# Kernel optimization log

Hardware: AMD Instinct MI355X
Metric: run time of the kernel (lower is better)

## Reference

```python
import jax, jax.numpy as jnp
import numpy as np

B, N, C, W = 128, 512, 128, 128
MASK_FILL = -1e-06  # faithful to original (sic: -1e-06, not -1e6)


def setup_inputs() -> dict:
    key = jax.random.key(0)
    ks = jax.random.split(key, 8)
    s = 1.0 / np.sqrt(C)
    return {
        "x": jax.random.normal(ks[0], (B, N, C), dtype=jnp.float32),
        "Wq": jax.random.normal(ks[1], (C, W), dtype=jnp.float32) * s,
        "bq": jnp.zeros((W,), dtype=jnp.float32),
        "Wk": jax.random.normal(ks[2], (C, W), dtype=jnp.float32) * s,
        "bk": jnp.zeros((W,), dtype=jnp.float32),
        "Wv": jax.random.normal(ks[3], (C, W), dtype=jnp.float32) * s,
        "bv": jnp.zeros((W,), dtype=jnp.float32),
        "valid_len": jax.random.randint(ks[4], (B,), 0, N, dtype=jnp.int64),
    }


def reference(x, Wq, bq, Wk, bk, Wv, bv, valid_len):
    # QKV projections: [B, N, W]
    q = jnp.einsum("bnc,cw->bnw", x, Wq) + bq
    k = jnp.einsum("bnc,cw->bnw", x, Wk) + bk
    v = jnp.einsum("bnc,cw->bnw", x, Wv) + bv
    # scores: [B, N, N]
    scores = jnp.einsum("bnw,bmw->bnm", q, k)
    # masked softmax: positions m where m > valid_len[b] get MASK_FILL
    # (mask is identical across query rows n since valid_len is per-batch)
    keep = jnp.arange(N)[None, None, :] <= valid_len[:, None, None]  # [B,1,N]
    scores = jnp.where(keep, scores, MASK_FILL)
    attn = jax.nn.softmax(scores, axis=-1)
    return jnp.einsum("bnm,bmw->bnw", attn, v)
```

## Files before the change

kernel.cpp:

```cpp
#include <hip/hip_runtime.h>
#include <hip/hip_fp16.h>
#include <math.h>

#define B_ 128
#define N_ 512
#define C_ 128
#define W_ 128
#define LDSW 136

typedef _Float16 f16;
typedef _Float16 f16x8 __attribute__((ext_vector_type(8)));
typedef _Float16 f16x4 __attribute__((ext_vector_type(4)));
typedef float f32x4 __attribute__((ext_vector_type(4)));

#define MFMA16(a, b, c) __builtin_amdgcn_mfma_f32_16x16x32_f16(a, b, c, 0, 0, 0)

#define LOG2E 1.44269504f
#define MASKF (-1e-6f * LOG2E)

static __device__ __forceinline__ f32x4 max4(f32x4 a, f32x4 b) {
  f32x4 r;
  r[0] = fmaxf(a[0], b[0]);
  r[1] = fmaxf(a[1], b[1]);
  r[2] = fmaxf(a[2], b[2]);
  r[3] = fmaxf(a[3], b[3]);
  return r;
}

__global__ __launch_bounds__(256) void prep_w(const float* __restrict__ Wq,
                                              const float* __restrict__ Wk,
                                              const float* __restrict__ Wv,
                                              f16* __restrict__ wT) {
  __shared__ float xs[16 * 129];
  const float* src = blockIdx.x == 0 ? Wq : (blockIdx.x == 1 ? Wk : Wv);
  f16* dst = wT + (size_t)blockIdx.x * C_ * W_;
  const int c0 = blockIdx.y * 16;
  const int t = threadIdx.x;
  for (int ii = 0; ii < 2; ++ii) {
    int idx = t + 256 * ii;
    int row = idx >> 5, w4 = idx & 31;
    float4 v = *reinterpret_cast<const float4*>(src + (c0 + row) * W_ + w4 * 4);
    xs[row * 129 + w4 * 4 + 0] = v.x;
    xs[row * 129 + w4 * 4 + 1] = v.y;
    xs[row * 129 + w4 * 4 + 2] = v.z;
    xs[row * 129 + w4 * 4 + 3] = v.w;
  }
  __syncthreads();
  int o = t * 8;
  int w = o >> 4, cc = o & 15;
  f16x8 h;
  for (int jj = 0; jj < 8; ++jj) h[jj] = (f16)xs[(cc + jj) * 129 + w];
  *reinterpret_cast<f16x8*>(dst + w * C_ + c0 + cc) = h;
}

__global__ __launch_bounds__(256, 2) void proj(const float* __restrict__ x,
                                               const float* __restrict__ bq,
                                               const float* __restrict__ bk,
                                               const float* __restrict__ bv,
                                               const f16* __restrict__ wT,
                                               f16* __restrict__ q,
                                               f16* __restrict__ k,
                                               f16* __restrict__ vT) {
  __shared__ f16 wls[2][128 * LDSW];
  const int b = blockIdx.y, n0 = blockIdx.x * 128;
  const int t = threadIdx.x, wave = t >> 6, lane = t & 63;
  const int quad = lane >> 4, l15 = lane & 15;

  float4 xr[2][4][2];
  for (int tile = 0; tile < 2; ++tile)
    for (int ks = 0; ks < 4; ++ks) {
      const float* p = x + ((size_t)(b * N_ + n0 + wave * 32 + tile * 16 +
                                     l15)) * C_ + ks * 32 + quad * 8;
      xr[tile][ks][0] = *reinterpret_cast<const float4*>(p);
      xr[tile][ks][1] = *reinterpret_cast<const float4*>(p + 4);
    }

  for (int i = 0; i < 8; ++i) {
    int idx = t + 256 * i;
    f16x8 tmp = *reinterpret_cast<const f16x8*>(wT + (size_t)idx * 8);
    *reinterpret_cast<f16x8*>(&wls[0][(idx >> 4) * LDSW + (idx & 15) * 8]) =
        tmp;
  }

  f16x8 af[2][4];
  for (int tile = 0; tile < 2; ++tile)
    for (int ks = 0; ks < 4; ++ks) {
      f16x8 h;
      h[0] = (f16)xr[tile][ks][0].x; h[1] = (f16)xr[tile][ks][0].y;
      h[2] = (f16)xr[tile][ks][0].z; h[3] = (f16)xr[tile][ks][0].w;
      h[4] = (f16)xr[tile][ks][1].x; h[5] = (f16)xr[tile][ks][1].y;
      h[6] = (f16)xr[tile][ks][1].z; h[7] = (f16)xr[tile][ks][1].w;
      af[tile][ks] = h;
    }
  __syncthreads();

  for (int ph = 0; ph < 3; ++ph) {
    const f16* wl = wls[ph & 1];

    f16x8 wst[8];
    if (ph < 2)
      for (int i = 0; i < 8; ++i)
        wst[i] = *reinterpret_cast<const f16x8*>(
            wT + (size_t)(ph + 1) * 16384 + (size_t)(t + 256 * i) * 8);

    f32x4 acc[8][2];
    for (int ct = 0; ct < 8; ++ct) {
      acc[ct][0] = {0.f, 0.f, 0.f, 0.f};
      acc[ct][1] = {0.f, 0.f, 0.f, 0.f};
    }

    if (ph < 2) {
      for (int ct = 0; ct < 8; ++ct) {
        f16x8 wf[4];
        for (int ks = 0; ks < 4; ++ks)
          wf[ks] = *reinterpret_cast<const f16x8*>(
              &wl[(ct * 16 + l15) * LDSW + ks * 32 + quad * 8]);
        for (int ks = 0; ks < 4; ++ks) {
          acc[ct][0] = MFMA16(wf[ks], af[0][ks], acc[ct][0]);
          acc[ct][1] = MFMA16(wf[ks], af[1][ks], acc[ct][1]);
        }
      }
      const float* bias = ph == 0 ? bq : bk;
      const float scale = ph == 0 ? LOG2E : 1.0f;
      f16* dst = ph == 0 ? q : k;
      for (int ct = 0; ct < 8; ++ct) {
        const float4 bb =
            *reinterpret_cast<const float4*>(bias + ct * 16 + quad * 4);
        for (int tile = 0; tile < 2; ++tile) {
          int n = n0 + wave * 32 + tile * 16 + l15;
          f16x4 h;
          h.x = (f16)((acc[ct][tile][0] + bb.x) * scale);
          h.y = (f16)((acc[ct][tile][1] + bb.y) * scale);
          h.z = (f16)((acc[ct][tile][2] + bb.z) * scale);
          h.w = (f16)((acc[ct][tile][3] + bb.w) * scale);
          *reinterpret_cast<f16x4*>(dst + ((size_t)(b * N_ + n)) * W_ +
                                    ct * 16 + quad * 4) = h;
        }
      }
    } else {
      for (int ct = 0; ct < 8; ++ct) {
        f16x8 wf[4];
        for (int ks = 0; ks < 4; ++ks)
          wf[ks] = *reinterpret_cast<const f16x8*>(
              &wl[(ct * 16 + l15) * LDSW + ks * 32 + quad * 8]);
        for (int ks = 0; ks < 4; ++ks) {
          acc[ct][0] = MFMA16(af[0][ks], wf[ks], acc[ct][0]);
          acc[ct][1] = MFMA16(af[1][ks], wf[ks], acc[ct][1]);
        }
      }
      for (int ct = 0; ct < 8; ++ct) {
        int wcol = ct * 16 + l15;
        float bb = bv[wcol];
        for (int tile = 0; tile < 2; ++tile) {
          int n = n0 + wave * 32 + tile * 16 + quad * 4;
          f16x4 h;
          h.x = (f16)(acc[ct][tile][0] + bb);
          h.y = (f16)(acc[ct][tile][1] + bb);
          h.z = (f16)(acc[ct][tile][2] + bb);
          h.w = (f16)(acc[ct][tile][3] + bb);
          *reinterpret_cast<f16x4*>(&vT[((size_t)(b * W_ + wcol)) * N_ + n]) =
              h;
        }
      }
    }

    if (ph < 2) {
      for (int i = 0; i < 8; ++i) {
        int idx = t + 256 * i;
        *reinterpret_cast<f16x8*>(
            &wls[(ph + 1) & 1][(idx >> 4) * LDSW + (idx & 15) * 8]) = wst[i];
      }
      __syncthreads();
    }
  }
}

__global__ __launch_bounds__(256, 2) void flash(const f16* __restrict__ q,
                                                const f16* __restrict__ k,
                                                const f16* __restrict__ vT,
                                                const int* __restrict__ vlen,
                                                float* __restrict__ out) {
  __shared__ f16 kls[128 * LDSW];
  __shared__ f16 pls[128 * LDSW];
  __shared__ float bcast[128];
  const int b = blockIdx.x, m0 = blockIdx.y * 128;
  const int t = threadIdx.x, wave = t >> 6, lane = t & 63;
  const int quad = lane >> 4, l15 = lane & 15;
  const int vl = vlen[b];
  const int mcol = m0 + wave * 32;
  const int srow = t >> 4, sc16 = t & 15;

  f16x8 qf[2][4];
  for (int ct = 0; ct < 2; ++ct)
    for (int kt = 0; kt < 4; ++kt)
      qf[ct][kt] = *reinterpret_cast<const f16x8*>(
          q + ((size_t)(b * N_ + mcol + ct * 16 + l15)) * W_ + kt * 32 +
          quad * 8);

  f32x4 oacc[2][8];
  for (int wt = 0; wt < 2; ++wt)
    for (int cm = 0; cm < 8; ++cm) oacc[wt][cm] = {0.f, 0.f, 0.f, 0.f};
  float mrun[2] = {-3.4e38f, -3.4e38f}, lrun[2] = {0.f, 0.f};

  for (int i = 0; i < 8; ++i) {
    int row = srow + 16 * i;
    f16x8 tmp = *reinterpret_cast<const f16x8*>(
        k + ((size_t)(b * N_ + row)) * W_ + sc16 * 8);
    *reinterpret_cast<f16x8*>(&kls[row * LDSW + sc16 * 8]) = tmp;
  }
  __syncthreads();

  for (int j = 0; j < 4; ++j) {
    const int n0 = j * 128;
    const int rel = vl - n0;

    f16x8 vfa[4];
    for (int kt = 0; kt < 4; ++kt)
      vfa[kt] = *reinterpret_cast<const f16x8*>(
          vT + ((size_t)(b * W_ + wave * 32 + l15)) * N_ + n0 + kt * 32 +
          quad * 8);

    f16x8 kst[8];
    if (j < 3)
      for (int i = 0; i < 8; ++i)
        kst[i] = *reinterpret_cast<const f16x8*>(
            k + ((size_t)(b * N_ + n0 + 128 + srow + 16 * i)) * W_ + sc16 * 8);

    f32x4 sacc[8][2];
    for (int i = 0; i < 8; ++i) {
      sacc[i][0] = {0.f, 0.f, 0.f, 0.f};
      sacc[i][1] = {0.f, 0.f, 0.f, 0.f};
      f16x8 kf[4];
      for (int kt = 0; kt < 4; ++kt)
        kf[kt] = *reinterpret_cast<const f16x8*>(
            &kls[(i * 16 + l15) * LDSW + kt * 32 + quad * 8]);
      for (int kt = 0; kt < 4; ++kt) {
        sacc[i][0] = MFMA16(kf[kt], qf[0][kt], sacc[i][0]);
        sacc[i][1] = MFMA16(kf[kt], qf[1][kt], sacc[i][1]);
      }
    }

    if (rel >= 0 && rel < 128) {
#pragma unroll
      for (int i = 0; i < 8; ++i) {
        if (rel >= 16 * i && rel < 16 * i + 15) {
          for (int r = 0; r < 4; ++r) {
            int nn = 16 * i + quad * 4 + r;
            if (nn > rel) { sacc[i][0][r] = MASKF; sacc[i][1][r] = MASKF; }
          }
        }
      }
    }

    float alpha[2];
    for (int ct = 0; ct < 2; ++ct) {
      f32x4 vmx = {-3.4e38f, -3.4e38f, -3.4e38f, -3.4e38f};
#pragma unroll
      for (int i = 0; i < 8; ++i)
        if (16 * i <= rel) vmx = max4(vmx, sacc[i][ct]);
      float mx = fmaxf(fmaxf(vmx[0], vmx[1]), fmaxf(vmx[2], vmx[3]));
      mx = fmaxf(mx, __shfl_xor(mx, 16));
      mx = fmaxf(mx, __shfl_xor(mx, 32));
      float mnew = fmaxf(mrun[ct], mx);
      alpha[ct] = exp2f(mrun[ct] - mnew);
      mrun[ct] = mnew;
      float pm = exp2f(MASKF - mnew);
      f32x4 vs = {0.f, 0.f, 0.f, 0.f};
      float sm = 0.f;
#pragma unroll
      for (int i = 0; i < 8; ++i) {
        if (16 * i > rel) {
          f32x4 v = {pm, pm, pm, pm};
          sacc[i][ct] = v;
          sm += 4.f * pm;
        } else {
          for (int r = 0; r < 4; ++r)
            sacc[i][ct][r] = exp2f(sacc[i][ct][r] - mnew);
          vs += sacc[i][ct];
        }
      }
      float s = (vs[0] + vs[1]) + (vs[2] + vs[3]) + sm;
      s += __shfl_xor(s, 16);
      s += __shfl_xor(s, 32);
      lrun[ct] = lrun[ct] * alpha[ct] + s;
    }

    for (int i = 0; i < 8; ++i)
      for (int ct = 0; ct < 2; ++ct) {
        f16x4 h;
        h.x = (f16)sacc[i][ct][0];
        h.y = (f16)sacc[i][ct][1];
        h.z = (f16)sacc[i][ct][2];
        h.w = (f16)sacc[i][ct][3];
        *reinterpret_cast<f16x4*>(
            &pls[(wave * 32 + ct * 16 + l15) * LDSW + 16 * i + quad * 4]) = h;
      }
    if (quad == 0) {
      bcast[wave * 32 + l15] = alpha[0];
      bcast[wave * 32 + 16 + l15] = alpha[1];
    }

    f16x8 vfb[4];
    for (int kt = 0; kt < 4; ++kt)
      vfb[kt] = *reinterpret_cast<const f16x8*>(
          vT + ((size_t)(b * W_ + wave * 32 + 16 + l15)) * N_ + n0 + kt * 32 +
          quad * 8);
    __syncthreads();

    if (j < 3)
      for (int i = 0; i < 8; ++i)
        *reinterpret_cast<f16x8*>(&kls[(srow + 16 * i) * LDSW + sc16 * 8]) =
            kst[i];

    float al[8];
    for (int cm = 0; cm < 8; ++cm) al[cm] = bcast[cm * 16 + l15];
    for (int wt = 0; wt < 2; ++wt)
      for (int cm = 0; cm < 8; ++cm) oacc[wt][cm] *= al[cm];
    for (int cm = 0; cm < 8; ++cm) {
      f16x8 pf[4];
      for (int kt = 0; kt < 4; ++kt)
        pf[kt] = *reinterpret_cast<const f16x8*>(
            &pls[(cm * 16 + l15) * LDSW + kt * 32 + quad * 8]);
      for (int kt = 0; kt < 4; ++kt) {
        oacc[0][cm] = MFMA16(vfa[kt], pf[kt], oacc[0][cm]);
        oacc[1][cm] = MFMA16(vfb[kt], pf[kt], oacc[1][cm]);
      }
    }
    __syncthreads();
  }

  if (quad == 0) {
    bcast[wave * 32 + l15] = 1.f / lrun[0];
    bcast[wave * 32 + 16 + l15] = 1.f / lrun[1];
  }
  __syncthreads();
  for (int cm = 0; cm < 8; ++cm) {
    float inv = bcast[cm * 16 + l15];
    int m = m0 + cm * 16 + l15;
    for (int wt = 0; wt < 2; ++wt) {
      int w = wave * 32 + wt * 16 + quad * 4;
      float4 o;
      o.x = oacc[wt][cm][0] * inv;
      o.y = oacc[wt][cm][1] * inv;
      o.z = oacc[wt][cm][2] * inv;
      o.w = oacc[wt][cm][3] * inv;
      *reinterpret_cast<float4*>(&out[((size_t)(b * N_ + m)) * W_ + w]) = o;
    }
  }
}

extern "C" void kernel_launch(void* const* d_in, const int* in_sizes, int n_in,
                              void* d_out, int out_size, void* d_ws,
                              size_t ws_size, hipStream_t stream) {
  const float* x  = (const float*)d_in[0];
  const float* Wq = (const float*)d_in[1];
  const float* bq = (const float*)d_in[2];
  const float* Wk = (const float*)d_in[3];
  const float* bk = (const float*)d_in[4];
  const float* Wv = (const float*)d_in[5];
  const float* bv = (const float*)d_in[6];
  const int* vlen = (const int*)d_in[7];
  float* out = (float*)d_out;

  char* ws = (char*)d_ws;
  f16* wT = (f16*)ws;
  f16* q  = (f16*)(ws + (1u << 20));
  f16* k  = (f16*)(ws + (1u << 20) + (16u << 20));
  f16* vT = (f16*)(ws + (1u << 20) + (32u << 20));

  prep_w<<<dim3(3, 8), 256, 0, stream>>>(Wq, Wk, Wv, wT);
  proj<<<dim3(4, 128), 256, 0, stream>>>(x, bq, bk, bv, wT, q, k, vT);
  flash<<<dim3(128, 4), 256, 0, stream>>>(q, k, vT, vlen, out);
}
```

Before: 143.0 us.

## Load K fragments directly from global memory instead of staging through LDS

Removes the shared-memory K tile and its cooperative staging and prefetch, and instead has each wave load its K MFMA fragments straight from global memory, double-buffered one 16-row tile ahead in registers. Freeing the K LDS buffer cuts shared memory per block, and the launch bound is raised from 2 to 3 blocks per CU to use that. The cost is that all four waves now redundantly read the same K rows from global/L2, and the higher occupancy target may force register spills given the large oacc/sacc register footprint.

```diff
diff --git a/kernel.cpp b/kernel.cpp
--- a/kernel.cpp
+++ b/kernel.cpp
@@ -175,12 +175,11 @@
   }
 }
 
-__global__ __launch_bounds__(256, 2) void flash(const f16* __restrict__ q,
+__global__ __launch_bounds__(256, 3) void flash(const f16* __restrict__ q,
                                                 const f16* __restrict__ k,
                                                 const f16* __restrict__ vT,
                                                 const int* __restrict__ vlen,
                                                 float* __restrict__ out) {
-  __shared__ f16 kls[128 * LDSW];
   __shared__ f16 pls[128 * LDSW];
   __shared__ float bcast[128];
   const int b = blockIdx.x, m0 = blockIdx.y * 128;
@@ -188,7 +187,6 @@
   const int quad = lane >> 4, l15 = lane & 15;
   const int vl = vlen[b];
   const int mcol = m0 + wave * 32;
-  const int srow = t >> 4, sc16 = t & 15;
 
   f16x8 qf[2][4];
   for (int ct = 0; ct < 2; ++ct)
@@ -202,17 +200,11 @@
     for (int cm = 0; cm < 8; ++cm) oacc[wt][cm] = {0.f, 0.f, 0.f, 0.f};
   float mrun[2] = {-3.4e38f, -3.4e38f}, lrun[2] = {0.f, 0.f};
 
-  for (int i = 0; i < 8; ++i) {
-    int row = srow + 16 * i;
-    f16x8 tmp = *reinterpret_cast<const f16x8*>(
-        k + ((size_t)(b * N_ + row)) * W_ + sc16 * 8);
-    *reinterpret_cast<f16x8*>(&kls[row * LDSW + sc16 * 8]) = tmp;
-  }
-  __syncthreads();
-
   for (int j = 0; j < 4; ++j) {
     const int n0 = j * 128;
     const int rel = vl - n0;
+    const f16* kb =
+        k + ((size_t)(b * N_ + n0 + l15)) * W_ + quad * 8;
 
     f16x8 vfa[4];
     for (int kt = 0; kt < 4; ++kt)
@@ -220,24 +212,23 @@
           vT + ((size_t)(b * W_ + wave * 32 + l15)) * N_ + n0 + kt * 32 +
           quad * 8);
 
-    f16x8 kst[8];
-    if (j < 3)
-      for (int i = 0; i < 8; ++i)
-        kst[i] = *reinterpret_cast<const f16x8*>(
-            k + ((size_t)(b * N_ + n0 + 128 + srow + 16 * i)) * W_ + sc16 * 8);
-
     f32x4 sacc[8][2];
+    f16x8 kfA[4], kfB[4];
+    for (int kt = 0; kt < 4; ++kt)
+      kfA[kt] = *reinterpret_cast<const f16x8*>(kb + kt * 32);
+#pragma unroll
     for (int i = 0; i < 8; ++i) {
+      if (i < 7)
+        for (int kt = 0; kt < 4; ++kt)
+          kfB[kt] = *reinterpret_cast<const f16x8*>(
+              kb + (size_t)(i + 1) * 16 * W_ + kt * 32);
       sacc[i][0] = {0.f, 0.f, 0.f, 0.f};
       sacc[i][1] = {0.f, 0.f, 0.f, 0.f};
-      f16x8 kf[4];
-      for (int kt = 0; kt < 4; ++kt)
-        kf[kt] = *reinterpret_cast<const f16x8*>(
-            &kls[(i * 16 + l15) * LDSW + kt * 32 + quad * 8]);
       for (int kt = 0; kt < 4; ++kt) {
-        sacc[i][0] = MFMA16(kf[kt], qf[0][kt], sacc[i][0]);
-        sacc[i][1] = MFMA16(kf[kt], qf[1][kt], sacc[i][1]);
-      }
+        sacc[i][0] = MFMA16(kfA[kt], qf[0][kt], sacc[i][0]);
+        sacc[i][1] = MFMA16(kfA[kt], qf[1][kt], sacc[i][1]);
+      }
+      for (int kt = 0; kt < 4; ++kt) kfA[kt] = kfB[kt];
     }
 
     if (rel >= 0 && rel < 128) {
@@ -307,11 +298,6 @@
           quad * 8);
     __syncthreads();
 
-    if (j < 3)
-      for (int i = 0; i < 8; ++i)
-        *reinterpret_cast<f16x8*>(&kls[(srow + 16 * i) * LDSW + sc16 * 8]) =
-            kst[i];
-
     float al[8];
     for (int cm = 0; cm < 8; ++cm) al[cm] = bcast[cm * 16 + l15];
     for (int wt = 0; wt < 2; ++wt)
```

New measurement: 194.4 us. 1.36x slower.

## Halve flash query tile to 64 rows to double grid and raise occupancy

Applied to the files above, without the earlier changes.

The flash kernel now handles 64 query rows per block instead of 128, with each wave owning 16 rows, and the grid grows from 128x4 to 128x8 blocks. Per-thread accumulators and P-tile LDS shrink, so launch bounds can ask for 3 blocks per CU. This is meant to improve occupancy and load balance across CUs. In exchange, every K and V tile is loaded and staged by twice as many blocks, which raises global and LDS traffic per useful MFMA.

```diff
diff --git a/kernel.cpp b/kernel.cpp
--- a/kernel.cpp
+++ b/kernel.cpp
@@ -175,32 +175,30 @@
   }
 }
 
-__global__ __launch_bounds__(256, 2) void flash(const f16* __restrict__ q,
+__global__ __launch_bounds__(256, 3) void flash(const f16* __restrict__ q,
                                                 const f16* __restrict__ k,
                                                 const f16* __restrict__ vT,
                                                 const int* __restrict__ vlen,
                                                 float* __restrict__ out) {
   __shared__ f16 kls[128 * LDSW];
-  __shared__ f16 pls[128 * LDSW];
-  __shared__ float bcast[128];
-  const int b = blockIdx.x, m0 = blockIdx.y * 128;
+  __shared__ f16 pls[64 * LDSW];
+  __shared__ float bcast[64];
+  const int b = blockIdx.x, m0 = blockIdx.y * 64;
   const int t = threadIdx.x, wave = t >> 6, lane = t & 63;
   const int quad = lane >> 4, l15 = lane & 15;
   const int vl = vlen[b];
-  const int mcol = m0 + wave * 32;
+  const int mcol = m0 + wave * 16;
   const int srow = t >> 4, sc16 = t & 15;
 
-  f16x8 qf[2][4];
-  for (int ct = 0; ct < 2; ++ct)
-    for (int kt = 0; kt < 4; ++kt)
-      qf[ct][kt] = *reinterpret_cast<const f16x8*>(
-          q + ((size_t)(b * N_ + mcol + ct * 16 + l15)) * W_ + kt * 32 +
-          quad * 8);
-
-  f32x4 oacc[2][8];
+  f16x8 qf[4];
+  for (int kt = 0; kt < 4; ++kt)
+    qf[kt] = *reinterpret_cast<const f16x8*>(
+        q + ((size_t)(b * N_ + mcol + l15)) * W_ + kt * 32 + quad * 8);
+
+  f32x4 oacc[2][4];
   for (int wt = 0; wt < 2; ++wt)
-    for (int cm = 0; cm < 8; ++cm) oacc[wt][cm] = {0.f, 0.f, 0.f, 0.f};
-  float mrun[2] = {-3.4e38f, -3.4e38f}, lrun[2] = {0.f, 0.f};
+    for (int cm = 0; cm < 4; ++cm) oacc[wt][cm] = {0.f, 0.f, 0.f, 0.f};
+  float mrun = -3.4e38f, lrun = 0.f;
 
   for (int i = 0; i < 8; ++i) {
     int row = srow + 16 * i;
@@ -226,18 +224,15 @@
         kst[i] = *reinterpret_cast<const f16x8*>(
             k + ((size_t)(b * N_ + n0 + 128 + srow + 16 * i)) * W_ + sc16 * 8);
 
-    f32x4 sacc[8][2];
+    f32x4 sacc[8];
     for (int i = 0; i < 8; ++i) {
-      sacc[i][0] = {0.f, 0.f, 0.f, 0.f};
-      sacc[i][1] = {0.f, 0.f, 0.f, 0.f};
+      sacc[i] = {0.f, 0.f, 0.f, 0.f};
       f16x8 kf[4];
       for (int kt = 0; kt < 4; ++kt)
         kf[kt] = *reinterpret_cast<const f16x8*>(
             &kls[(i * 16 + l15) * LDSW + kt * 32 + quad * 8]);
-      for (int kt = 0; kt < 4; ++kt) {
-        sacc[i][0] = MFMA16(kf[kt], qf[0][kt], sacc[i][0]);
-        sacc[i][1] = MFMA16(kf[kt], qf[1][kt], sacc[i][1]);
-      }
+      for (int kt = 0; kt < 4; ++kt)
+        sacc[i] = MFMA16(kf[kt], qf[kt], sacc[i]);
     }
 
     if (rel >= 0 && rel < 128) {
@@ -246,24 +241,24 @@
         if (rel >= 16 * i && rel < 16 * i + 15) {
           for (int r = 0; r < 4; ++r) {
             int nn = 16 * i + quad * 4 + r;
-            if (nn > rel) { sacc[i][0][r] = MASKF; sacc[i][1][r] = MASKF; }
+            if (nn > rel) sacc[i][r] = MASKF;
           }
         }
       }
     }
 
-    float alpha[2];
-    for (int ct = 0; ct < 2; ++ct) {
+    float alpha;
+    {
       f32x4 vmx = {-3.4e38f, -3.4e38f, -3.4e38f, -3.4e38f};
 #pragma unroll
       for (int i = 0; i < 8; ++i)
-        if (16 * i <= rel) vmx = max4(vmx, sacc[i][ct]);
+        if (16 * i <= rel) vmx = max4(vmx, sacc[i]);
       float mx = fmaxf(fmaxf(vmx[0], vmx[1]), fmaxf(vmx[2], vmx[3]));
       mx = fmaxf(mx, __shfl_xor(mx, 16));
       mx = fmaxf(mx, __shfl_xor(mx, 32));
-      float mnew = fmaxf(mrun[ct], mx);
-      alpha[ct] = exp2f(mrun[ct] - mnew);
-      mrun[ct] = mnew;
+      float mnew = fmaxf(mrun, mx);
+      alpha = exp2f(mrun - mnew);
+      mrun = mnew;
       float pm = exp2f(MASKF - mnew);
       f32x4 vs = {0.f, 0.f, 0.f, 0.f};
       float sm = 0.f;
@@ -271,34 +266,30 @@
       for (int i = 0; i < 8; ++i) {
         if (16 * i > rel) {
           f32x4 v = {pm, pm, pm, pm};
-          sacc[i][ct] = v;
+          sacc[i] = v;
           sm += 4.f * pm;
         } else {
           for (int r = 0; r < 4; ++r)
-            sacc[i][ct][r] = exp2f(sacc[i][ct][r] - mnew);
-          vs += sacc[i][ct];
+            sacc[i][r] = exp2f(sacc[i][r] - mnew);
+          vs += sacc[i];
         }
       }
       float s = (vs[0] + vs[1]) + (vs[2] + vs[3]) + sm;
       s += __shfl_xor(s, 16);
       s += __shfl_xor(s, 32);
-      lrun[ct] = lrun[ct] * alpha[ct] + s;
-    }
-
-    for (int i = 0; i < 8; ++i)
-      for (int ct = 0; ct < 2; ++ct) {
-        f16x4 h;
-        h.x = (f16)sacc[i][ct][0];
-        h.y = (f16)sacc[i][ct][1];
-        h.z = (f16)sacc[i][ct][2];
-        h.w = (f16)sacc[i][ct][3];
-        *reinterpret_cast<f16x4*>(
-            &pls[(wave * 32 + ct * 16 + l15) * LDSW + 16 * i + quad * 4]) = h;
-      }
-    if (quad == 0) {
-      bcast[wave * 32 + l15] = alpha[0];
-      bcast[wave * 32 + 16 + l15] = alpha[1];
-    }
+      lrun = lrun * alpha + s;
+    }
+
+    for (int i = 0; i < 8; ++i) {
+      f16x4 h;
+      h.x = (f16)sacc[i][0];
+      h.y = (f16)sacc[i][1];
+      h.z = (f16)sacc[i][2];
+      h.w = (f16)sacc[i][3];
+      *reinterpret_cast<f16x4*>(
+          &pls[(wave * 16 + l15) * LDSW + 16 * i + quad * 4]) = h;
+    }
+    if (quad == 0) bcast[wave * 16 + l15] = alpha;
 
     f16x8 vfb[4];
     for (int kt = 0; kt < 4; ++kt)
@@ -312,11 +303,11 @@
         *reinterpret_cast<f16x8*>(&kls[(srow + 16 * i) * LDSW + sc16 * 8]) =
             kst[i];
 
-    float al[8];
-    for (int cm = 0; cm < 8; ++cm) al[cm] = bcast[cm * 16 + l15];
+    float al[4];
+    for (int cm = 0; cm < 4; ++cm) al[cm] = bcast[cm * 16 + l15];
     for (int wt = 0; wt < 2; ++wt)
-      for (int cm = 0; cm < 8; ++cm) oacc[wt][cm] *= al[cm];
-    for (int cm = 0; cm < 8; ++cm) {
+      for (int cm = 0; cm < 4; ++cm) oacc[wt][cm] *= al[cm];
+    for (int cm = 0; cm < 4; ++cm) {
       f16x8 pf[4];
       for (int kt = 0; kt < 4; ++kt)
         pf[kt] = *reinterpret_cast<const f16x8*>(
@@ -329,12 +320,9 @@
     __syncthreads();
   }
 
-  if (quad == 0) {
-    bcast[wave * 32 + l15] = 1.f / lrun[0];
-    bcast[wave * 32 + 16 + l15] = 1.f / lrun[1];
-  }
+  if (quad == 0) bcast[wave * 16 + l15] = 1.f / lrun;
   __syncthreads();
-  for (int cm = 0; cm < 8; ++cm) {
+  for (int cm = 0; cm < 4; ++cm) {
     float inv = bcast[cm * 16 + l15];
     int m = m0 + cm * 16 + l15;
     for (int wt = 0; wt < 2; ++wt) {
@@ -370,5 +358,5 @@
 
   prep_w<<<dim3(3, 8), 256, 0, stream>>>(Wq, Wk, Wv, wT);
   proj<<<dim3(4, 128), 256, 0, stream>>>(x, bq, bk, bv, wT, q, k, vT);
-  flash<<<dim3(128, 4), 256, 0, stream>>>(q, k, vT, vlen, out);
-}
+  flash<<<dim3(128, 8), 256, 0, stream>>>(q, k, vT, vlen, out);
+}
```

Measured after the change: 183.4 us. +28.2%, slower.
